# Performance work log

Hardware: AMD Instinct MI355X
Metric: run time of the kernel (lower is better)

Reference implementation:

```python
import jax, jax.numpy as jnp
import numpy as np

B, N, D, S, H = 64, 4096, 256, 8, 512
ITERS = 3
EPS = 1e-8
SCALE = D ** -0.5
LN_EPS = 1e-5


def _ln(x, w, b):
    mu = jnp.mean(x, axis=-1, keepdims=True)
    var = jnp.var(x, axis=-1, keepdims=True)
    return (x - mu) * jax.lax.rsqrt(var + LN_EPS) * w + b


def setup_inputs() -> dict:
    key = jax.random.key(0)
    ks = jax.random.split(key, 20)
    g = lambda k, shape, s=0.02: jax.random.normal(k, shape, dtype=jnp.float32) * s
    return {
        "inputs": jax.random.normal(ks[0], (B, N, D), dtype=jnp.float32),
        "query_pos": jax.random.uniform(ks[1], (1, S, D), dtype=jnp.float32),
        "wq": g(ks[2], (D, D)), "bq": jnp.zeros((D,), jnp.float32),
        "wk": g(ks[3], (D, D)), "bk": jnp.zeros((D,), jnp.float32),
        "wv": g(ks[4], (D, D)), "bv": jnp.zeros((D,), jnp.float32),
        "w_ih": g(ks[5], (3 * D, D)), "b_ih": jnp.zeros((3 * D,), jnp.float32),
        "w_hh": g(ks[6], (3 * D, D)), "b_hh": jnp.zeros((3 * D,), jnp.float32),
        "w1": g(ks[7], (H, D)), "b1": jnp.zeros((H,), jnp.float32),
        "w2": g(ks[8], (D, H)), "b2": jnp.zeros((D,), jnp.float32),
        "ln_in_w": jnp.ones((D,), jnp.float32), "ln_in_b": jnp.zeros((D,), jnp.float32),
        "ln_s_w": jnp.ones((D,), jnp.float32), "ln_s_b": jnp.zeros((D,), jnp.float32),
        "ln_ff_w": jnp.ones((D,), jnp.float32), "ln_ff_b": jnp.zeros((D,), jnp.float32),
    }


def _step(slots, k, v, wq, bq, w_ih, b_ih, w_hh, b_hh, w1, b1, w2, b2,
          ln_s_w, ln_s_b, ln_ff_w, ln_ff_b):
    s = _ln(slots, ln_s_w, ln_s_b)
    q = s @ wq.T + bq                                  # [B,S,D]
    dots = jnp.einsum('bid,bjd->bij', q, k) * SCALE    # [B,S,N]
    attn = jax.nn.softmax(dots, axis=1) + EPS          # softmax over slots
    attn = attn / jnp.sum(attn, axis=-1, keepdims=True)
    updates = jnp.einsum('bjd,bij->bid', v, attn)      # [B,S,D]
    # GRUCell(input=updates, hidden=slots), PyTorch gate order r,z,n
    gx = updates @ w_ih.T + b_ih
    gh = slots @ w_hh.T + b_hh
    xr, xz, xn = jnp.split(gx, 3, axis=-1)
    hr, hz, hn = jnp.split(gh, 3, axis=-1)
    r = jax.nn.sigmoid(xr + hr)
    z = jax.nn.sigmoid(xz + hz)
    n = jnp.tanh(xn + r * hn)
    h = (1.0 - z) * n + z * slots
    ff = jnp.maximum(_ln(h, ln_ff_w, ln_ff_b) @ w1.T + b1, 0.0) @ w2.T + b2
    return h + ff


def reference(inputs, query_pos, wq, bq, wk, bk, wv, bv,
              w_ih, b_ih, w_hh, b_hh, w1, b1, w2, b2,
              ln_in_w, ln_in_b, ln_s_w, ln_s_b, ln_ff_w, ln_ff_b):
    b = inputs.shape[0]
    slots = jnp.broadcast_to(query_pos, (b, S, D))
    x = _ln(inputs, ln_in_w, ln_in_b)
    k = x @ wk.T + bk
    v = x @ wv.T + bv
    step = lambda s: _step(s, k, v, wq, bq, w_ih, b_ih, w_hh, b_hh,
                           w1, b1, w2, b2, ln_s_w, ln_s_b, ln_ff_w, ln_ff_b)
    for _ in range(ITERS):
        slots = step(slots)
    slots = step(jax.lax.stop_gradient(slots))
    return slots
```

## Files before the change

### kernel.cpp

```cpp
#include <hip/hip_runtime.h>
#include <hip/hip_bf16.h>

#define DEV __device__ __forceinline__
typedef unsigned short u16;
using s16x8  = __attribute__((ext_vector_type(8))) short;
using f32x4v = __attribute__((ext_vector_type(4))) float;

constexpr float SCALE  = 0.0625f;
constexpr float EPS    = 1e-8f;
constexpr float LN_EPS = 1e-5f;

DEV u16 f2bf(float f) {
    __hip_bfloat16 h = __float2bfloat16(f);
    u16 u; __builtin_memcpy(&u, &h, 2); return u;
}
DEV float bf2f(u16 u) {
    unsigned int x = ((unsigned int)u) << 16;
    float f; __builtin_memcpy(&f, &x, 4); return f;
}
DEV float ld1(const void* p, size_t i, int bf) {
    return bf ? bf2f(((const u16*)p)[i]) : ((const float*)p)[i];
}
DEV float warp_sum64(float v) {
    v += __shfl_xor(v, 1);  v += __shfl_xor(v, 2);  v += __shfl_xor(v, 4);
    v += __shfl_xor(v, 8);  v += __shfl_xor(v, 16); v += __shfl_xor(v, 32);
    return v;
}
DEV float sigf(float x) { return 1.f / (1.f + expf(-x)); }

__global__ void k_sniff(const void* __restrict__ x, int* __restrict__ flag) {
    int lane = threadIdx.x;
    u16 u = ((const u16*)x)[lane * 2];
    float v = bf2f(u);
    bool bad = !(fabsf(v) <= 1024.0f);
    unsigned long long m = __ballot(bad);
    if (lane == 0) *flag = (m == 0ull) ? 1 : 0;
}

__global__ __launch_bounds__(256) void k_prep_misc(
    const void* bq, const void* bk, const void* bv, const void* bih, const void* bhh,
    const void* b1, const void* b2, const void* liw, const void* lib,
    const void* lsw, const void* lsb, const void* lfw, const void* lfb,
    float* o_bq, float* o_bk, float* o_bv, float* o_bih, float* o_bhh,
    float* o_b1, float* o_b2, float* o_liw, float* o_lib,
    float* o_lsw, float* o_lsb, float* o_lfw, float* o_lfb,
    const int* flagp) {
    int bf = *flagp;
    int i = blockIdx.x * 256 + threadIdx.x;
    if (i < 256) { o_bq[i]  = ld1(bq,  i, bf); return; } i -= 256;
    if (i < 256) { o_bk[i]  = ld1(bk,  i, bf); return; } i -= 256;
    if (i < 256) { o_bv[i]  = ld1(bv,  i, bf); return; } i -= 256;
    if (i < 768) { o_bih[i] = ld1(bih, i, bf); return; } i -= 768;
    if (i < 768) { o_bhh[i] = ld1(bhh, i, bf); return; } i -= 768;
    if (i < 512) { o_b1[i]  = ld1(b1,  i, bf); return; } i -= 512;
    if (i < 256) { o_b2[i]  = ld1(b2,  i, bf); return; } i -= 256;
    if (i < 256) { o_liw[i] = ld1(liw, i, bf); return; } i -= 256;
    if (i < 256) { o_lib[i] = ld1(lib, i, bf); return; } i -= 256;
    if (i < 256) { o_lsw[i] = ld1(lsw, i, bf); return; } i -= 256;
    if (i < 256) { o_lsb[i] = ld1(lsb, i, bf); return; } i -= 256;
    if (i < 256) { o_lfw[i] = ld1(lfw, i, bf); return; } i -= 256;
    if (i < 256) { o_lfb[i] = ld1(lfb, i, bf); }
}

__global__ __launch_bounds__(256) void k_prep_w(
    const void* wq, const void* wv, const void* wk,
    const void* wih, const void* whh, const void* w1, const void* w2,
    u16* wqT_b, u16* wvT_b, u16* wk2_b, u16* wih_b, u16* whh_b, u16* w1_b, u16* w2_b,
    const float* __restrict__ liw, const int* flagp) {
    int bf = *flagp;
    int i = blockIdx.x * 256 + threadIdx.x;
    if (i < 65536)  { int c=i>>8, d=i&255; wqT_b[i] = f2bf(ld1(wq, (size_t)d*256+c, bf)); return; } i -= 65536;
    if (i < 65536)  { int c=i>>8, d=i&255; wvT_b[i] = f2bf(ld1(wv, (size_t)d*256+c, bf)); return; } i -= 65536;
    if (i < 65536)  { int n=i>>8, d=i&255; wk2_b[i] = f2bf(ld1(wk, (size_t)d*256+n, bf) * liw[n]); return; } i -= 65536;
    if (i < 196608) { wih_b[i] = f2bf(ld1(wih, i, bf)); return; } i -= 196608;
    if (i < 196608) { whh_b[i] = f2bf(ld1(whh, i, bf)); return; } i -= 196608;
    if (i < 131072) { w1_b[i]  = f2bf(ld1(w1,  i, bf)); return; } i -= 131072;
    if (i < 131072) { w2_b[i]  = f2bf(ld1(w2,  i, bf)); }
}

__global__ __launch_bounds__(256) void k_prep_m(const void* __restrict__ wk,
    const float* __restrict__ liw, const float* __restrict__ lib,
    const float* __restrict__ bk_f, float* __restrict__ m1p, float* __restrict__ m2p,
    const int* flagp) {
    int bf = *flagp;
    int wave = threadIdx.x >> 6, lane = threadIdx.x & 63;
    int d = blockIdx.x * 4 + wave;
    float s1 = 0.f, s2 = 0.f;
#pragma unroll
    for (int t = 0; t < 4; t++) {
        int c = lane * 4 + t;
        float w = ld1(wk, (size_t)d * 256 + c, bf);
        s1 += w * lib[c];
        s2 += w * liw[c];
    }
    s1 = warp_sum64(s1); s2 = warp_sum64(s2);
    if (lane == 0) { m1p[d] = s1 + bk_f[d]; m2p[d] = -s2; }
}

__global__ __launch_bounds__(256) void k_prep_u(
    const void* __restrict__ wq, const void* __restrict__ wk, const void* __restrict__ wih,
    const float* __restrict__ m1p, const float* __restrict__ m2p,
    const float* __restrict__ bq_f, const float* __restrict__ bv_f,
    const float* __restrict__ liw,
    float* __restrict__ u1, float* __restrict__ u2, float* __restrict__ bq2,
    float* __restrict__ wibv, float* __restrict__ c12, const int* flagp) {
    int bf = *flagp;
    int wave = threadIdx.x >> 6, lane = threadIdx.x & 63;
    int idx = blockIdx.x * 4 + wave;
    if (idx >= 1538) return;
    float s = 0.f;
#pragma unroll
    for (int t = 0; t < 4; t++) {
        int d = lane * 4 + t;
        if (idx < 256)       s += ld1(wq, (size_t)d*256 + idx, bf) * m1p[d];
        else if (idx < 512)  s += ld1(wq, (size_t)d*256 + (idx-256), bf) * m2p[d];
        else if (idx < 768)  s += bq_f[d] * ld1(wk, (size_t)d*256 + (idx-512), bf);
        else if (idx < 1536) s += ld1(wih, (size_t)(idx-768)*256 + d, bf) * bv_f[d];
        else if (idx == 1536) s += bq_f[d] * m1p[d];
        else                  s += bq_f[d] * m2p[d];
    }
    s = warp_sum64(s);
    if (lane == 0) {
        if (idx < 256)       u1[idx] = s;
        else if (idx < 512)  u2[idx-256] = s;
        else if (idx < 768)  bq2[idx-512] = s * liw[idx-512];
        else if (idx < 1536) wibv[idx-768] = s;
        else                 c12[idx-1536] = s;
    }
}

__global__ __launch_bounds__(256) void k_conv(const void* __restrict__ x,
    u16* __restrict__ XB, u16* __restrict__ XT,
    float* __restrict__ mu, float* __restrict__ rs, const int* flagp) {
    int bf = *flagp;
    int jt = blockIdx.x;
    int b  = blockIdx.y;
    int tid = threadIdx.x;
    __shared__ __attribute__((aligned(16))) u16 LT[64 * 264];
    int jr   = tid >> 5;
    int cseg = tid & 31;
#pragma unroll
    for (int it = 0; it < 8; ++it) {
        int j = it * 8 + jr;
        size_t rowg = (size_t)b * 4096 + (size_t)jt * 64 + j;
        s16x8 val;
        float v[8];
        if (bf) {
            val = *(const s16x8*)((const u16*)x + rowg * 256 + cseg * 8);
#pragma unroll
            for (int e = 0; e < 8; e++) v[e] = bf2f((u16)val[e]);
        } else {
            const float4* sf = (const float4*)((const float*)x + rowg * 256 + cseg * 8);
            float4 f0 = sf[0], f1 = sf[1];
            v[0]=f0.x; v[1]=f0.y; v[2]=f0.z; v[3]=f0.w;
            v[4]=f1.x; v[5]=f1.y; v[6]=f1.z; v[7]=f1.w;
#pragma unroll
            for (int e = 0; e < 8; e++) val[e] = (short)f2bf(v[e]);
            *(s16x8*)(XB + rowg * 256 + cseg * 8) = val;
        }
        *(s16x8*)(LT + j * 264 + cseg * 8) = val;
        float ps = 0.f, ps2 = 0.f;
#pragma unroll
        for (int e = 0; e < 8; e++) { ps += v[e]; ps2 += v[e] * v[e]; }
        ps  += __shfl_xor(ps, 1);  ps  += __shfl_xor(ps, 2);  ps  += __shfl_xor(ps, 4);
        ps  += __shfl_xor(ps, 8);  ps  += __shfl_xor(ps, 16);
        ps2 += __shfl_xor(ps2, 1); ps2 += __shfl_xor(ps2, 2); ps2 += __shfl_xor(ps2, 4);
        ps2 += __shfl_xor(ps2, 8); ps2 += __shfl_xor(ps2, 16);
        if (cseg == 0) {
            float m = ps * (1.f / 256.f);
            mu[rowg] = m;
            rs[rowg] = rsqrtf(ps2 * (1.f / 256.f) - m * m + LN_EPS);
        }
    }
    __syncthreads();
    int c = tid;
    u16* dst = XT + ((size_t)b * 256 + c) * 4096 + (size_t)jt * 64;
#pragma unroll
    for (int k = 0; k < 8; ++k) {
        s16x8 o;
#pragma unroll
        for (int t = 0; t < 8; t++) o[t] = (short)LT[(k * 8 + t) * 264 + c];
        *(s16x8*)(dst + k * 8) = o;
    }
}

__global__ __launch_bounds__(256) void k_prep_s(const void* __restrict__ qp,
    const float* __restrict__ lsw, const float* __restrict__ lsb,
    const float* __restrict__ u1, const float* __restrict__ u2, const float* __restrict__ c12,
    float* __restrict__ slots, u16* __restrict__ Acat, u16* __restrict__ s_b,
    float* __restrict__ kap, float* __restrict__ lam, const int* flagp) {
    int bf = *flagp;
    int m = blockIdx.x;
    int s_ = m & 7, d = threadIdx.x;
    float v = ld1(qp, (size_t)s_ * 256 + d, bf);
    slots[(size_t)m*256 + d]   = v;
    Acat[(size_t)m*512 + 256 + d] = f2bf(v);
    __shared__ float red[16];
    float su = warp_sum64(v), sq = warp_sum64(v*v);
    int wave = threadIdx.x >> 6, lane = threadIdx.x & 63;
    if (lane == 0) { red[wave] = su; red[4+wave] = sq; }
    __syncthreads();
    float S1 = red[0]+red[1]+red[2]+red[3], S2 = red[4]+red[5]+red[6]+red[7];
    float muv = S1*(1.f/256.f);
    float rsv = rsqrtf(S2*(1.f/256.f) - muv*muv + LN_EPS);
    float sn = (v - muv)*rsv*lsw[d] + lsb[d];
    s_b[(size_t)m*256 + d] = f2bf(sn);
    float ks = warp_sum64(sn * u1[d]), ls = warp_sum64(sn * u2[d]);
    if (lane == 0) { red[8+wave] = ks; red[12+wave] = ls; }
    __syncthreads();
    if (threadIdx.x == 0) {
        kap[m] = red[8]+red[9]+red[10]+red[11] + c12[0];
        lam[m] = red[12]+red[13]+red[14]+red[15] + c12[1];
    }
}

template<bool OUT_BF16, bool RELU>
__global__ __launch_bounds__(256) void gemm64(
    const u16* __restrict__ A, const u16* __restrict__ W,
    const float* __restrict__ bias, void* __restrict__ outp, int Nn, int K) {
    int m0 = blockIdx.x * 64, n0 = blockIdx.y * 64;
    int tid = threadIdx.x;
    int wave = tid >> 6, lane = tid & 63, quad = lane >> 4, l15 = lane & 15;
    int wm = wave >> 1, wn = wave & 1;
    __shared__ __attribute__((aligned(16))) u16 A_s[64*40];
    __shared__ __attribute__((aligned(16))) u16 B_s[64*40];
    f32x4v acc[2][2];
#pragma unroll
    for (int i = 0; i < 2; i++)
#pragma unroll
        for (int j = 0; j < 2; j++) acc[i][j] = (f32x4v){0.f,0.f,0.f,0.f};
    int r0 = tid >> 2, seg = tid & 3;
    int nkc = K >> 5;
    for (int kc = 0; kc < nkc; ++kc) {
        s16x8 a0 = *(const s16x8*)(A + (size_t)(m0 + r0)*K + kc*32 + seg*8);
        s16x8 b0 = *(const s16x8*)(W + (size_t)(n0 + r0)*K + kc*32 + seg*8);
        __syncthreads();
        *(s16x8*)(A_s + r0*40 + seg*8) = a0;
        *(s16x8*)(B_s + r0*40 + seg*8) = b0;
        __syncthreads();
        s16x8 af[2], bfr[2];
#pragma unroll
        for (int t = 0; t < 2; t++) af[t]  = *(const s16x8*)(A_s + (wm*32 + t*16 + l15)*40 + quad*8);
#pragma unroll
        for (int t = 0; t < 2; t++) bfr[t] = *(const s16x8*)(B_s + (wn*32 + t*16 + l15)*40 + quad*8);
#pragma unroll
        for (int ti = 0; ti < 2; ti++)
#pragma unroll
            for (int tj = 0; tj < 2; tj++)
                acc[ti][tj] = __builtin_amdgcn_mfma_f32_16x16x32_bf16(af[ti], bfr[tj], acc[ti][tj], 0, 0, 0);
    }
#pragma unroll
    for (int tj = 0; tj < 2; tj++) {
        int colg = n0 + wn*32 + tj*16 + l15;
        float bv_ = bias ? bias[colg] : 0.f;
#pragma unroll
        for (int ti = 0; ti < 2; ti++) {
            int rowb = m0 + wm*32 + ti*16 + quad*4;
#pragma unroll
            for (int r = 0; r < 4; r++) {
                float v = acc[ti][tj][r] + bv_;
                if (RELU) v = fmaxf(v, 0.f);
                if (OUT_BF16) ((u16*)outp)[(size_t)(rowb + r)*Nn + colg] = f2bf(v);
                else          ((float*)outp)[(size_t)(rowb + r)*Nn + colg] = v;
            }
        }
    }
}

__global__ __launch_bounds__(256) void k_big(const u16* __restrict__ Wc2_b,
    const u16* __restrict__ whh_b, const float* __restrict__ bih_f,
    const float* __restrict__ bhh_f, const float* __restrict__ wibv,
    u16* __restrict__ Wbig, float* __restrict__ bbig) {
    int idx = blockIdx.x * 256 + threadIdx.x;
    int n = idx >> 9, k = idx & 511;
    u16 v;
    if (n < 512)      v = (k < 256) ? Wc2_b[(size_t)n*256 + k] : whh_b[(size_t)n*256 + (k-256)];
    else if (n < 768) v = (k < 256) ? Wc2_b[(size_t)n*256 + k] : (u16)0;
    else              v = (k < 256) ? (u16)0 : whh_b[(size_t)(n-256)*256 + (k-256)];
    Wbig[idx] = v;
    if (idx < 1024) {
        float bb;
        if (idx < 512)      bb = bih_f[idx] + wibv[idx] + bhh_f[idx];
        else if (idx < 768) bb = bih_f[idx] + wibv[idx];
        else                bb = bhh_f[idx-256];
        bbig[idx] = bb;
    }
}

__global__ __launch_bounds__(256) void k_attn(
    const void* __restrict__ xraw, const u16* __restrict__ XB,
    const u16* __restrict__ XT, const u16* __restrict__ q2b,
    const float* __restrict__ kap, const float* __restrict__ lam,
    const float* __restrict__ mu, const float* __restrict__ rs,
    const int* __restrict__ flagp,
    float* __restrict__ Zp, float* __restrict__ Rp, float* __restrict__ Tp) {
    int bf = *flagp;
    const u16* xb = bf ? (const u16*)xraw : XB;
    int jcc = blockIdx.x;
    int b   = blockIdx.y;
    int tid = threadIdx.x;
    int wave = tid >> 6, lane = tid & 63, quad = lane >> 4, l15 = lane & 15;
    __shared__ __attribute__((aligned(16))) u16 q_s[16*264];
    __shared__ __attribute__((aligned(16))) u16 a_s[2][16*72];
    __shared__ float kl_s[32];
    {
        int row = tid >> 5, seg = tid & 31;
        s16x8 qv = *(const s16x8*)(q2b + (size_t)(b*8 + row)*256 + seg*8);
        *(s16x8*)(q_s + row*264 + seg*8) = qv;
        s16x8 z = {0,0,0,0,0,0,0,0};
        *(s16x8*)(q_s + (8+row)*264 + seg*8) = z;
    }
    if (tid < 16) {
        kl_s[tid]      = (tid < 8) ? kap[b*8 + tid] : 0.f;
        kl_s[16 + tid] = (tid < 8) ? lam[b*8 + tid] : 0.f;
    }
    __syncthreads();

    f32x4v accz[4];
#pragma unroll
    for (int t = 0; t < 4; t++) accz[t] = (f32x4v){0.f,0.f,0.f,0.f};
    float rtot[4] = {0.f,0.f,0.f,0.f}, ttot[4] = {0.f,0.f,0.f,0.f};
    int jb16 = wave * 16;
    const u16* xtb = XT + (size_t)b * 256 * 4096;

    for (int sub = 0; sub < 2; ++sub) {
        int jloc = (jcc*2 + sub) * 64;
        size_t rowg = (size_t)b*4096 + jloc + jb16 + l15;
        const u16* xbp = xb + rowg*256 + quad*8;
        s16x8 xv[8];
#pragma unroll
        for (int kc = 0; kc < 8; ++kc) xv[kc] = *(const s16x8*)(xbp + kc*32);
        f32x4v accd = (f32x4v){0.f,0.f,0.f,0.f};
#pragma unroll
        for (int kc = 0; kc < 8; ++kc) {
            s16x8 af = *(const s16x8*)(q_s + l15*264 + kc*32 + quad*8);
            accd = __builtin_amdgcn_mfma_f32_16x16x32_bf16(af, xv[kc], accd, 0, 0, 0);
        }
        s16x8 zv[8];
#pragma unroll
        for (int ct = 0; ct < 4; ++ct) {
            int c = wave*64 + ct*16 + l15;
#pragma unroll
            for (int kc2 = 0; kc2 < 2; ++kc2)
                zv[ct*2 + kc2] = *(const s16x8*)(xtb + (size_t)c*4096 + jloc + kc2*32 + quad*8);
        }
        float rsj = rs[rowg], mrj = mu[rowg] * rsj;
        float dv[4];
#pragma unroll
        for (int r = 0; r < 4; r++)
            dv[r] = SCALE*(rsj*accd[r] + mrj*kl_s[16 + quad*4 + r] + kl_s[quad*4 + r]);
        float mx = fmaxf(fmaxf(dv[0], dv[1]), fmaxf(dv[2], dv[3]));
        mx = fmaxf(mx, __shfl_xor(mx, 16));
        float ev[4];
        float sum = 0.f;
#pragma unroll
        for (int r = 0; r < 4; r++) { ev[r] = expf(dv[r] - mx); sum += ev[r]; }
        sum += __shfl_xor(sum, 16);
        float inv = 1.f / sum;
#pragma unroll
        for (int r = 0; r < 4; r++) {
            float a = ev[r]*inv + EPS;
            rtot[r] += a;
            ttot[r] += a * mrj;
            a_s[sub][(quad*4 + r)*72 + jb16 + l15] = f2bf(a * rsj);
        }
        __syncthreads();
#pragma unroll
        for (int ct = 0; ct < 4; ++ct) {
#pragma unroll
            for (int kc2 = 0; kc2 < 2; ++kc2) {
                s16x8 af2 = *(const s16x8*)(a_s[sub] + l15*72 + kc2*32 + quad*8);
                accz[ct] = __builtin_amdgcn_mfma_f32_16x16x32_bf16(af2, zv[ct*2 + kc2], accz[ct], 0, 0, 0);
            }
        }
    }
    if (quad < 2) {
#pragma unroll
        for (int ct = 0; ct < 4; ++ct) {
            int c = wave*64 + ct*16 + l15;
#pragma unroll
            for (int r = 0; r < 4; r++)
                Zp[((size_t)(b*32 + jcc)*8 + quad*4 + r)*256 + c] = accz[ct][r];
        }
    }
#pragma unroll
    for (int r = 0; r < 4; r++) {
        rtot[r] += __shfl_xor(rtot[r], 1);
        rtot[r] += __shfl_xor(rtot[r], 2);
        rtot[r] += __shfl_xor(rtot[r], 4);
        rtot[r] += __shfl_xor(rtot[r], 8);
        ttot[r] += __shfl_xor(ttot[r], 1);
        ttot[r] += __shfl_xor(ttot[r], 2);
        ttot[r] += __shfl_xor(ttot[r], 4);
        ttot[r] += __shfl_xor(ttot[r], 8);
    }
    if (l15 == 0 && quad < 2) {
        int base = ((b*32 + jcc)*4 + wave)*8 + quad*4;
#pragma unroll
        for (int r = 0; r < 4; r++) { Rp[base + r] = rtot[r]; Tp[base + r] = ttot[r]; }
    }
}

__global__ __launch_bounds__(256) void k_reduce(const float* __restrict__ Zp,
    const float* __restrict__ Rp, const float* __restrict__ Tp,
    const float* __restrict__ liw, const float* __restrict__ lib,
    u16* __restrict__ Acat) {
    int m = blockIdx.x;
    int b = m >> 3, i = m & 7, d = threadIdx.x;
    float z = 0.f;
#pragma unroll
    for (int c = 0; c < 32; c++) z += Zp[((size_t)(b*32 + c)*8 + i)*256 + d];
    float rv = 0.f, tv = 0.f;
    if (d < 128) {
        rv = Rp[(size_t)(b*128 + d)*8 + i];
        tv = Tp[(size_t)(b*128 + d)*8 + i];
    }
    __shared__ float redR[4], redT[4];
    rv = warp_sum64(rv); tv = warp_sum64(tv);
    int wave = d >> 6, lane = d & 63;
    if (lane == 0) { redR[wave] = rv; redT[wave] = tv; }
    __syncthreads();
    float R = redR[0]+redR[1]+redR[2]+redR[3];
    float T = redT[0]+redT[1]+redT[2]+redT[3];
    float ys = (liw[d]*(z - T) + lib[d]*R) / R;
    Acat[(size_t)m*512 + d] = f2bf(ys);
}

__global__ __launch_bounds__(256) void k_gates(const float* __restrict__ g,
    const float* __restrict__ slots, const float* __restrict__ lfw,
    const float* __restrict__ lfb, float* __restrict__ h, u16* __restrict__ hln_b) {
    int m = blockIdx.x, d = threadIdx.x;
    const float* gm = g + (size_t)m*1024;
    float r = sigf(gm[d]);
    float z = sigf(gm[256 + d]);
    float nn = tanhf(gm[512 + d] + r * gm[768 + d]);
    float hv = (1.f - z)*nn + z*slots[(size_t)m*256 + d];
    h[(size_t)m*256 + d] = hv;
    __shared__ float red[8];
    float su = warp_sum64(hv), sq = warp_sum64(hv*hv);
    int wave = threadIdx.x >> 6, lane = threadIdx.x & 63;
    if (lane == 0) { red[wave] = su; red[4+wave] = sq; }
    __syncthreads();
    float S1 = red[0]+red[1]+red[2]+red[3], S2 = red[4]+red[5]+red[6]+red[7];
    float muv = S1*(1.f/256.f);
    float rsv = rsqrtf(S2*(1.f/256.f) - muv*muv + LN_EPS);
    hln_b[(size_t)m*256 + d] = f2bf((hv - muv)*rsv*lfw[d] + lfb[d]);
}

__global__ __launch_bounds__(256) void k_residual(const float* __restrict__ h,
    const float* __restrict__ ff2, const float* __restrict__ lsw,
    const float* __restrict__ lsb, const float* __restrict__ u1,
    const float* __restrict__ u2, const float* __restrict__ c12,
    float* __restrict__ slots, u16* __restrict__ Acat, u16* __restrict__ s_b,
    float* __restrict__ kap, float* __restrict__ lam) {
    int m = blockIdx.x, d = threadIdx.x;
    float sv = h[(size_t)m*256 + d] + ff2[(size_t)m*256 + d];
    slots[(size_t)m*256 + d] = sv;
    Acat[(size_t)m*512 + 256 + d] = f2bf(sv);
    __shared__ float red[16];
    float su = warp_sum64(sv), sq = warp_sum64(sv*sv);
    int wave = threadIdx.x >> 6, lane = threadIdx.x & 63;
    if (lane == 0) { red[wave] = su; red[4+wave] = sq; }
    __syncthreads();
    float S1 = red[0]+red[1]+red[2]+red[3], S2 = red[4]+red[5]+red[6]+red[7];
    float muv = S1*(1.f/256.f);
    float rsv = rsqrtf(S2*(1.f/256.f) - muv*muv + LN_EPS);
    float sn = (sv - muv)*rsv*lsw[d] + lsb[d];
    s_b[(size_t)m*256 + d] = f2bf(sn);
    float ks = warp_sum64(sn * u1[d]), ls = warp_sum64(sn * u2[d]);
    if (lane == 0) { red[8+wave] = ks; red[12+wave] = ls; }
    __syncthreads();
    if (threadIdx.x == 0) {
        kap[m] = red[8]+red[9]+red[10]+red[11] + c12[0];
        lam[m] = red[12]+red[13]+red[14]+red[15] + c12[1];
    }
}

__global__ __launch_bounds__(256) void k_out(const float* __restrict__ slots,
                                             void* __restrict__ out, const int* flagp) {
    int bf = *flagp;
    int i = blockIdx.x * 256 + threadIdx.x;
    if (bf) ((u16*)out)[i] = f2bf(slots[i]);
    else    ((float*)out)[i] = slots[i];
}

extern "C" void kernel_launch(void* const* d_in, const int* in_sizes, int n_in,
                              void* d_out, int out_size, void* d_ws, size_t ws_size,
                              hipStream_t stream) {
    (void)in_sizes; (void)n_in; (void)out_size; (void)ws_size;
    const void* inputs    = d_in[0];
    const void* query_pos = d_in[1];
    const void* wq   = d_in[2];  const void* bq   = d_in[3];
    const void* wk   = d_in[4];  const void* bk   = d_in[5];
    const void* wv   = d_in[6];  const void* bv   = d_in[7];
    const void* w_ih = d_in[8];  const void* b_ih = d_in[9];
    const void* w_hh = d_in[10]; const void* b_hh = d_in[11];
    const void* w1   = d_in[12]; const void* b1   = d_in[13];
    const void* w2   = d_in[14]; const void* b2   = d_in[15];
    const void* ln_in_w = d_in[16]; const void* ln_in_b = d_in[17];
    const void* ln_s_w  = d_in[18]; const void* ln_s_b  = d_in[19];
    const void* ln_ff_w = d_in[20]; const void* ln_ff_b = d_in[21];

    char* w = (char*)d_ws;
    size_t off = 0;
    auto alloc = [&](size_t bytes) -> void* {
        void* p = w + off;
        off = (off + bytes + 255) & ~(size_t)255;
        return p;
    };
    u16*   XB     = (u16*)alloc(134217728);
    u16*   XT     = (u16*)alloc(134217728);
    float* Zp     = (float*)alloc(16777216);
    float* gates  = (float*)alloc(2097152);
    u16*   Wbig_b = (u16*)alloc(1048576);
    u16*   Wc2_b  = (u16*)alloc(393216);
    u16*   Wc_b   = (u16*)alloc(131072);
    u16*   wqT_b  = (u16*)alloc(131072);
    u16*   wvT_b  = (u16*)alloc(131072);
    u16*   wk2_b  = (u16*)alloc(131072);
    u16*   wih_b  = (u16*)alloc(393216);
    u16*   whh_b  = (u16*)alloc(393216);
    u16*   w1_b   = (u16*)alloc(262144);
    u16*   w2_b   = (u16*)alloc(262144);
    float* mu     = (float*)alloc(1048576);
    float* rs     = (float*)alloc(1048576);
    float* slots  = (float*)alloc(524288);
    u16*   s_b    = (u16*)alloc(262144);
    u16*   Acat   = (u16*)alloc(524288);
    u16*   q2_b   = (u16*)alloc(262144);
    float* h      = (float*)alloc(524288);
    u16*   hln_b  = (u16*)alloc(262144);
    u16*   ff1_b  = (u16*)alloc(524288);
    float* ff2    = (float*)alloc(524288);
    float* Rp     = (float*)alloc(262144);
    float* Tp     = (float*)alloc(262144);
    float* bq_f   = (float*)alloc(1024);
    float* bk_f   = (float*)alloc(1024);
    float* bv_f   = (float*)alloc(1024);
    float* bih_f  = (float*)alloc(3072);
    float* bhh_f  = (float*)alloc(3072);
    float* b1_f   = (float*)alloc(2048);
    float* b2_f   = (float*)alloc(1024);
    float* liw_f  = (float*)alloc(1024);
    float* lib_f  = (float*)alloc(1024);
    float* lsw_f  = (float*)alloc(1024);
    float* lsb_f  = (float*)alloc(1024);
    float* lfw_f  = (float*)alloc(1024);
    float* lfb_f  = (float*)alloc(1024);
    float* m1p    = (float*)alloc(1024);
    float* m2p    = (float*)alloc(1024);
    float* u1     = (float*)alloc(1024);
    float* u2     = (float*)alloc(1024);
    float* bq2    = (float*)alloc(1024);
    float* wibv   = (float*)alloc(3072);
    float* bbig   = (float*)alloc(4096);
    float* c12    = (float*)alloc(256);
    float* kap    = (float*)alloc(2048);
    float* lam    = (float*)alloc(2048);
    int*   flag   = (int*)alloc(256);

    k_sniff<<<1, 64, 0, stream>>>(inputs, flag);
    k_prep_misc<<<18, 256, 0, stream>>>(bq, bk, bv, b_ih, b_hh, b1, b2,
                                        ln_in_w, ln_in_b, ln_s_w, ln_s_b, ln_ff_w, ln_ff_b,
                                        bq_f, bk_f, bv_f, bih_f, bhh_f, b1_f, b2_f,
                                        liw_f, lib_f, lsw_f, lsb_f, lfw_f, lfb_f, flag);
    k_conv<<<dim3(64, 64), 256, 0, stream>>>(inputs, XB, XT, mu, rs, flag);
    k_prep_w<<<3328, 256, 0, stream>>>(wq, wv, wk, w_ih, w_hh, w1, w2,
                                       wqT_b, wvT_b, wk2_b, wih_b, whh_b, w1_b, w2_b,
                                       liw_f, flag);
    k_prep_m<<<64, 256, 0, stream>>>(wk, liw_f, lib_f, bk_f, m1p, m2p, flag);
    k_prep_u<<<385, 256, 0, stream>>>(wq, wk, w_ih, m1p, m2p, bq_f, bv_f, liw_f,
                                      u1, u2, bq2, wibv, c12, flag);
    k_prep_s<<<512, 256, 0, stream>>>(query_pos, lsw_f, lsb_f, u1, u2, c12,
                                      slots, Acat, s_b, kap, lam, flag);
    gemm64<true, false><<<dim3(4, 4), 256, 0, stream>>>(wk2_b, wqT_b, nullptr, Wc_b, 256, 256);
    gemm64<true, false><<<dim3(12, 4), 256, 0, stream>>>(wih_b, wvT_b, nullptr, Wc2_b, 256, 256);
    k_big<<<2048, 256, 0, stream>>>(Wc2_b, whh_b, bih_f, bhh_f, wibv, Wbig_b, bbig);

    for (int step = 0; step < 4; ++step) {
        gemm64<true, false><<<dim3(8, 4), 256, 0, stream>>>(s_b, Wc_b, bq2, q2_b, 256, 256);
        k_attn<<<dim3(32, 64), 256, 0, stream>>>(inputs, XB, XT, q2_b, kap, lam, mu, rs, flag, Zp, Rp, Tp);
        k_reduce<<<512, 256, 0, stream>>>(Zp, Rp, Tp, liw_f, lib_f, Acat);
        gemm64<false, false><<<dim3(8, 16), 256, 0, stream>>>(Acat, Wbig_b, bbig, gates, 1024, 512);
        k_gates<<<512, 256, 0, stream>>>(gates, slots, lfw_f, lfb_f, h, hln_b);
        gemm64<true, true ><<<dim3(8, 8), 256, 0, stream>>>(hln_b, w1_b, b1_f, ff1_b, 512, 256);
        gemm64<false, false><<<dim3(8, 4), 256, 0, stream>>>(ff1_b, w2_b, b2_f, ff2, 256, 512);
        k_residual<<<512, 256, 0, stream>>>(h, ff2, lsw_f, lsb_f, u1, u2, c12,
                                            slots, Acat, s_b, kap, lam);
    }
    k_out<<<512, 256, 0, stream>>>(slots, d_out, flag);
}
```

Measured before the change: 859.9 us.

## Fuse per-slot GRU, FFN, LayerNorm and query projection into one kernel

Replaces the gates GEMM, gate kernel, two FFN GEMMs, the residual kernel and the next step's q projection GEMM with a single k_slots kernel. Each block handles 16 slot rows and keeps intermediates in LDS and registers, doing the matmuls with MFMA. This removes five launches per iteration and the global round trips for gates, h, hln, ff1 and ff2. The cost is only 32 blocks, each streaming the full weight matrices from global/L2 without LDS tiling, so parallelism is low.

```diff
diff --git a/kernel.cpp b/kernel.cpp
--- a/kernel.cpp
+++ b/kernel.cpp
@@ -24,6 +24,11 @@
 DEV float warp_sum64(float v) {
     v += __shfl_xor(v, 1);  v += __shfl_xor(v, 2);  v += __shfl_xor(v, 4);
     v += __shfl_xor(v, 8);  v += __shfl_xor(v, 16); v += __shfl_xor(v, 32);
+    return v;
+}
+DEV float sum16(float v) {
+    v += __shfl_xor(v, 1); v += __shfl_xor(v, 2);
+    v += __shfl_xor(v, 4); v += __shfl_xor(v, 8);
     return v;
 }
 DEV float sigf(float x) { return 1.f / (1.f + expf(-x)); }
@@ -426,53 +431,195 @@
     Acat[(size_t)m*512 + d] = f2bf(ys);
 }
 
-__global__ __launch_bounds__(256) void k_gates(const float* __restrict__ g,
-    const float* __restrict__ slots, const float* __restrict__ lfw,
-    const float* __restrict__ lfb, float* __restrict__ h, u16* __restrict__ hln_b) {
-    int m = blockIdx.x, d = threadIdx.x;
-    const float* gm = g + (size_t)m*1024;
-    float r = sigf(gm[d]);
-    float z = sigf(gm[256 + d]);
-    float nn = tanhf(gm[512 + d] + r * gm[768 + d]);
-    float hv = (1.f - z)*nn + z*slots[(size_t)m*256 + d];
-    h[(size_t)m*256 + d] = hv;
-    __shared__ float red[8];
-    float su = warp_sum64(hv), sq = warp_sum64(hv*hv);
-    int wave = threadIdx.x >> 6, lane = threadIdx.x & 63;
-    if (lane == 0) { red[wave] = su; red[4+wave] = sq; }
-    __syncthreads();
-    float S1 = red[0]+red[1]+red[2]+red[3], S2 = red[4]+red[5]+red[6]+red[7];
-    float muv = S1*(1.f/256.f);
-    float rsv = rsqrtf(S2*(1.f/256.f) - muv*muv + LN_EPS);
-    hln_b[(size_t)m*256 + d] = f2bf((hv - muv)*rsv*lfw[d] + lfb[d]);
-}
-
-__global__ __launch_bounds__(256) void k_residual(const float* __restrict__ h,
-    const float* __restrict__ ff2, const float* __restrict__ lsw,
-    const float* __restrict__ lsb, const float* __restrict__ u1,
-    const float* __restrict__ u2, const float* __restrict__ c12,
-    float* __restrict__ slots, u16* __restrict__ Acat, u16* __restrict__ s_b,
-    float* __restrict__ kap, float* __restrict__ lam) {
-    int m = blockIdx.x, d = threadIdx.x;
-    float sv = h[(size_t)m*256 + d] + ff2[(size_t)m*256 + d];
-    slots[(size_t)m*256 + d] = sv;
-    Acat[(size_t)m*512 + 256 + d] = f2bf(sv);
-    __shared__ float red[16];
-    float su = warp_sum64(sv), sq = warp_sum64(sv*sv);
-    int wave = threadIdx.x >> 6, lane = threadIdx.x & 63;
-    if (lane == 0) { red[wave] = su; red[4+wave] = sq; }
-    __syncthreads();
-    float S1 = red[0]+red[1]+red[2]+red[3], S2 = red[4]+red[5]+red[6]+red[7];
-    float muv = S1*(1.f/256.f);
-    float rsv = rsqrtf(S2*(1.f/256.f) - muv*muv + LN_EPS);
-    float sn = (sv - muv)*rsv*lsw[d] + lsb[d];
-    s_b[(size_t)m*256 + d] = f2bf(sn);
-    float ks = warp_sum64(sn * u1[d]), ls = warp_sum64(sn * u2[d]);
-    if (lane == 0) { red[8+wave] = ks; red[12+wave] = ls; }
-    __syncthreads();
-    if (threadIdx.x == 0) {
-        kap[m] = red[8]+red[9]+red[10]+red[11] + c12[0];
-        lam[m] = red[12]+red[13]+red[14]+red[15] + c12[1];
+__global__ __launch_bounds__(256) void k_slots(
+    u16* __restrict__ Acat, float* __restrict__ slots,
+    const u16* __restrict__ Wbig, const float* __restrict__ bbig,
+    const u16* __restrict__ w1b, const float* __restrict__ b1f,
+    const u16* __restrict__ w2b, const float* __restrict__ b2f,
+    const u16* __restrict__ Wcb, const float* __restrict__ bq2,
+    const float* __restrict__ lfw, const float* __restrict__ lfb,
+    const float* __restrict__ lsw, const float* __restrict__ lsb,
+    const float* __restrict__ u1, const float* __restrict__ u2,
+    const float* __restrict__ c12,
+    float* __restrict__ kap, float* __restrict__ lam,
+    u16* __restrict__ q2b) {
+    int m0 = blockIdx.x * 16;
+    int tid = threadIdx.x;
+    int w = tid >> 6, lane = tid & 63, quad = lane >> 4, l15 = lane & 15;
+    __shared__ __attribute__((aligned(16))) u16 A_s[16*520];
+    __shared__ __attribute__((aligned(16))) u16 hln_s[16*264];
+    __shared__ __attribute__((aligned(16))) u16 ff1_s[16*520];
+    __shared__ __attribute__((aligned(16))) u16 sn_s[16*264];
+    __shared__ float red_a[4][16], red_b[4][16];
+
+#pragma unroll
+    for (int it = 0; it < 4; ++it) {
+        int chunk = it*256 + tid;
+        int row = chunk >> 6, seg = chunk & 63;
+        *(s16x8*)(A_s + row*520 + seg*8) =
+            *(const s16x8*)(Acat + (size_t)(m0 + row)*512 + seg*8);
+    }
+    __syncthreads();
+
+    float h_reg[4][4];
+    float su[4] = {0,0,0,0}, sq[4] = {0,0,0,0};
+#pragma unroll
+    for (int t = 0; t < 4; ++t) {
+        int nbase = w*64 + t*16 + l15;
+        int nr = nbase, nz = 256 + nbase, nn_ = 512 + nbase, nh = 768 + nbase;
+        f32x4v ar = (f32x4v){0,0,0,0}, az = (f32x4v){0,0,0,0};
+        f32x4v an = (f32x4v){0,0,0,0}, ah = (f32x4v){0,0,0,0};
+#pragma unroll
+        for (int kc = 0; kc < 16; ++kc) {
+            s16x8 af = *(const s16x8*)(A_s + l15*520 + kc*32 + quad*8);
+            s16x8 br = *(const s16x8*)(Wbig + (size_t)nr*512 + kc*32 + quad*8);
+            s16x8 bz = *(const s16x8*)(Wbig + (size_t)nz*512 + kc*32 + quad*8);
+            s16x8 bn = *(const s16x8*)(Wbig + (size_t)nn_*512 + kc*32 + quad*8);
+            s16x8 bh = *(const s16x8*)(Wbig + (size_t)nh*512 + kc*32 + quad*8);
+            ar = __builtin_amdgcn_mfma_f32_16x16x32_bf16(af, br, ar, 0, 0, 0);
+            az = __builtin_amdgcn_mfma_f32_16x16x32_bf16(af, bz, az, 0, 0, 0);
+            an = __builtin_amdgcn_mfma_f32_16x16x32_bf16(af, bn, an, 0, 0, 0);
+            ah = __builtin_amdgcn_mfma_f32_16x16x32_bf16(af, bh, ah, 0, 0, 0);
+        }
+        float br_ = bbig[nr], bz_ = bbig[nz], bn_ = bbig[nn_], bh_ = bbig[nh];
+        int d = w*64 + t*16 + l15;
+#pragma unroll
+        for (int r = 0; r < 4; ++r) {
+            int m = quad*4 + r;
+            float g_r = sigf(ar[r] + br_);
+            float g_z = sigf(az[r] + bz_);
+            float g_n = tanhf(an[r] + bn_ + g_r * (ah[r] + bh_));
+            float sold = slots[(size_t)(m0 + m)*256 + d];
+            float hv = (1.f - g_z)*g_n + g_z*sold;
+            h_reg[t][r] = hv;
+            su[r] += hv; sq[r] += hv*hv;
+        }
+    }
+#pragma unroll
+    for (int r = 0; r < 4; ++r) { su[r] = sum16(su[r]); sq[r] = sum16(sq[r]); }
+    if (l15 == 0) {
+#pragma unroll
+        for (int r = 0; r < 4; ++r) { red_a[w][quad*4 + r] = su[r]; red_b[w][quad*4 + r] = sq[r]; }
+    }
+    __syncthreads();
+    float muv[4], rsv[4];
+#pragma unroll
+    for (int r = 0; r < 4; ++r) {
+        int m = quad*4 + r;
+        float S1 = red_a[0][m] + red_a[1][m] + red_a[2][m] + red_a[3][m];
+        float S2 = red_b[0][m] + red_b[1][m] + red_b[2][m] + red_b[3][m];
+        muv[r] = S1 * (1.f/256.f);
+        rsv[r] = rsqrtf(S2 * (1.f/256.f) - muv[r]*muv[r] + LN_EPS);
+    }
+#pragma unroll
+    for (int t = 0; t < 4; ++t) {
+        int d = w*64 + t*16 + l15;
+        float lw = lfw[d], lb = lfb[d];
+#pragma unroll
+        for (int r = 0; r < 4; ++r) {
+            int m = quad*4 + r;
+            hln_s[m*264 + d] = f2bf((h_reg[t][r] - muv[r])*rsv[r]*lw + lb);
+        }
+    }
+    __syncthreads();
+
+#pragma unroll
+    for (int nt = 0; nt < 8; ++nt) {
+        int n = w*128 + nt*16 + l15;
+        f32x4v acc = (f32x4v){0,0,0,0};
+#pragma unroll
+        for (int kc = 0; kc < 8; ++kc) {
+            s16x8 af = *(const s16x8*)(hln_s + l15*264 + kc*32 + quad*8);
+            s16x8 bf = *(const s16x8*)(w1b + (size_t)n*256 + kc*32 + quad*8);
+            acc = __builtin_amdgcn_mfma_f32_16x16x32_bf16(af, bf, acc, 0, 0, 0);
+        }
+        float bv = b1f[n];
+#pragma unroll
+        for (int r = 0; r < 4; ++r)
+            ff1_s[(quad*4 + r)*520 + n] = f2bf(fmaxf(acc[r] + bv, 0.f));
+    }
+    __syncthreads();
+
+    float sv_reg[4][4];
+#pragma unroll
+    for (int r = 0; r < 4; ++r) { su[r] = 0.f; sq[r] = 0.f; }
+#pragma unroll
+    for (int nt = 0; nt < 4; ++nt) {
+        int n = w*64 + nt*16 + l15;
+        f32x4v acc = (f32x4v){0,0,0,0};
+#pragma unroll
+        for (int kc = 0; kc < 16; ++kc) {
+            s16x8 af = *(const s16x8*)(ff1_s + l15*520 + kc*32 + quad*8);
+            s16x8 bf = *(const s16x8*)(w2b + (size_t)n*512 + kc*32 + quad*8);
+            acc = __builtin_amdgcn_mfma_f32_16x16x32_bf16(af, bf, acc, 0, 0, 0);
+        }
+        float bv = b2f[n];
+#pragma unroll
+        for (int r = 0; r < 4; ++r) {
+            int m = quad*4 + r;
+            float sv = acc[r] + bv + h_reg[nt][r];
+            sv_reg[nt][r] = sv;
+            su[r] += sv; sq[r] += sv*sv;
+            slots[(size_t)(m0 + m)*256 + n] = sv;
+            Acat[(size_t)(m0 + m)*512 + 256 + n] = f2bf(sv);
+        }
+    }
+#pragma unroll
+    for (int r = 0; r < 4; ++r) { su[r] = sum16(su[r]); sq[r] = sum16(sq[r]); }
+    if (l15 == 0) {
+#pragma unroll
+        for (int r = 0; r < 4; ++r) { red_a[w][quad*4 + r] = su[r]; red_b[w][quad*4 + r] = sq[r]; }
+    }
+    __syncthreads();
+#pragma unroll
+    for (int r = 0; r < 4; ++r) {
+        int m = quad*4 + r;
+        float S1 = red_a[0][m] + red_a[1][m] + red_a[2][m] + red_a[3][m];
+        float S2 = red_b[0][m] + red_b[1][m] + red_b[2][m] + red_b[3][m];
+        muv[r] = S1 * (1.f/256.f);
+        rsv[r] = rsqrtf(S2 * (1.f/256.f) - muv[r]*muv[r] + LN_EPS);
+    }
+    __syncthreads();
+    float ks[4] = {0,0,0,0}, ls[4] = {0,0,0,0};
+#pragma unroll
+    for (int nt = 0; nt < 4; ++nt) {
+        int d = w*64 + nt*16 + l15;
+        float lw = lsw[d], lb = lsb[d], uu1 = u1[d], uu2 = u2[d];
+#pragma unroll
+        for (int r = 0; r < 4; ++r) {
+            int m = quad*4 + r;
+            float sn = (sv_reg[nt][r] - muv[r])*rsv[r]*lw + lb;
+            sn_s[m*264 + d] = f2bf(sn);
+            ks[r] += sn * uu1;
+            ls[r] += sn * uu2;
+        }
+    }
+#pragma unroll
+    for (int r = 0; r < 4; ++r) { ks[r] = sum16(ks[r]); ls[r] = sum16(ls[r]); }
+    if (l15 == 0) {
+#pragma unroll
+        for (int r = 0; r < 4; ++r) { red_a[w][quad*4 + r] = ks[r]; red_b[w][quad*4 + r] = ls[r]; }
+    }
+    __syncthreads();
+    if (tid < 16) {
+        int m = tid;
+        kap[m0 + m] = red_a[0][m] + red_a[1][m] + red_a[2][m] + red_a[3][m] + c12[0];
+        lam[m0 + m] = red_b[0][m] + red_b[1][m] + red_b[2][m] + red_b[3][m] + c12[1];
+    }
+#pragma unroll
+    for (int nt = 0; nt < 4; ++nt) {
+        int n = w*64 + nt*16 + l15;
+        f32x4v acc = (f32x4v){0,0,0,0};
+#pragma unroll
+        for (int kc = 0; kc < 8; ++kc) {
+            s16x8 af = *(const s16x8*)(sn_s + l15*264 + kc*32 + quad*8);
+            s16x8 bf = *(const s16x8*)(Wcb + (size_t)n*256 + kc*32 + quad*8);
+            acc = __builtin_amdgcn_mfma_f32_16x16x32_bf16(af, bf, acc, 0, 0, 0);
+        }
+        float bv = bq2[n];
+#pragma unroll
+        for (int r = 0; r < 4; ++r)
+            q2b[(size_t)(m0 + quad*4 + r)*256 + n] = f2bf(acc[r] + bv);
     }
 }
 
@@ -511,7 +658,6 @@
     u16*   XB     = (u16*)alloc(134217728);
     u16*   XT     = (u16*)alloc(134217728);
     float* Zp     = (float*)alloc(16777216);
-    float* gates  = (float*)alloc(2097152);
     u16*   Wbig_b = (u16*)alloc(1048576);
     u16*   Wc2_b  = (u16*)alloc(393216);
     u16*   Wc_b   = (u16*)alloc(131072);
@@ -528,10 +674,6 @@
     u16*   s_b    = (u16*)alloc(262144);
     u16*   Acat   = (u16*)alloc(524288);
     u16*   q2_b   = (u16*)alloc(262144);
-    float* h      = (float*)alloc(524288);
-    u16*   hln_b  = (u16*)alloc(262144);
-    u16*   ff1_b  = (u16*)alloc(524288);
-    float* ff2    = (float*)alloc(524288);
     float* Rp     = (float*)alloc(262144);
     float* Tp     = (float*)alloc(262144);
     float* bq_f   = (float*)alloc(1024);
@@ -576,17 +718,14 @@
     gemm64<true, false><<<dim3(4, 4), 256, 0, stream>>>(wk2_b, wqT_b, nullptr, Wc_b, 256, 256);
     gemm64<true, false><<<dim3(12, 4), 256, 0, stream>>>(wih_b, wvT_b, nullptr, Wc2_b, 256, 256);
     k_big<<<2048, 256, 0, stream>>>(Wc2_b, whh_b, bih_f, bhh_f, wibv, Wbig_b, bbig);
+    gemm64<true, false><<<dim3(8, 4), 256, 0, stream>>>(s_b, Wc_b, bq2, q2_b, 256, 256);
 
     for (int step = 0; step < 4; ++step) {
-        gemm64<true, false><<<dim3(8, 4), 256, 0, stream>>>(s_b, Wc_b, bq2, q2_b, 256, 256);
         k_attn<<<dim3(32, 64), 256, 0, stream>>>(inputs, XB, XT, q2_b, kap, lam, mu, rs, flag, Zp, Rp, Tp);
         k_reduce<<<512, 256, 0, stream>>>(Zp, Rp, Tp, liw_f, lib_f, Acat);
-        gemm64<false, false><<<dim3(8, 16), 256, 0, stream>>>(Acat, Wbig_b, bbig, gates, 1024, 512);
-        k_gates<<<512, 256, 0, stream>>>(gates, slots, lfw_f, lfb_f, h, hln_b);
-        gemm64<true, true ><<<dim3(8, 8), 256, 0, stream>>>(hln_b, w1_b, b1_f, ff1_b, 512, 256);
-        gemm64<false, false><<<dim3(8, 4), 256, 0, stream>>>(ff1_b, w2_b, b2_f, ff2, 256, 512);
-        k_residual<<<512, 256, 0, stream>>>(h, ff2, lsw_f, lsb_f, u1, u2, c12,
-                                            slots, Acat, s_b, kap, lam);
+        k_slots<<<32, 256, 0, stream>>>(Acat, slots, Wbig_b, bbig, w1_b, b1_f,
+                                        w2_b, b2_f, Wc_b, bq2, lfw_f, lfb_f,
+                                        lsw_f, lsb_f, u1, u2, c12, kap, lam, q2_b);
     }
     k_out<<<512, 256, 0, stream>>>(slots, d_out, flag);
 }
```

After: 990.0 us. 1.15x slower.
